# Kernel optimization log

Hardware: AMD Instinct MI355X
Metric: run time of the kernel (lower is better)

## Reference

```python
import jax, jax.numpy as jnp
import numpy as np

# Static config matching init_kwargs
COUT, CIN, K = 64, 64, 3
PAD = K // 2  # padding=1


def setup_inputs() -> dict:
    key = jax.random.key(0)
    k1, k2, k3 = jax.random.split(key, 3)
    B, H, W, FH, FW, SC = 2, 256, 256, 16, 16, 128
    hyper_params = COUT * CIN * K * K  # 36864
    x = jax.random.normal(k1, (B, CIN, H, W), jnp.float32)
    s = jax.random.normal(k2, (B, SC, FH, FW), jnp.float32)
    s2w = jax.random.normal(k3, (hyper_params, SC), jnp.float32) * 0.02
    return {"x": x, "s": s, "s2w": s2w}


def reference(x, s, s2w):
    """HyperPatchConv2d forward: per-patch dynamically generated 3x3 conv.

    x:   [b, c, h, w]   input feature map
    s:   [b, sc, fh, fw] hypernetwork signal (one vector per patch)
    s2w: [P, sc]         signal2weights 1x1 conv (P = out*cin*k*k)
    """
    b, c, h, w = x.shape
    fh, fw = s.shape[-2:]
    ph, pw = h // fh, w // fw          # patch size
    kh, kw = ph + 2 * PAD, pw + 2 * PAD  # unfold window (patch + halo)

    # signal2weights: 1x1 conv -> per-patch flattened conv weight
    wflat = jnp.einsum('pc,bcfg->bfgp', s2w, s)            # [b,fh,fw,P]
    Wdyn = wflat.reshape(b, fh, fw, COUT, CIN, K, K)        # per-patch conv kernels

    # reflect-pad then unfold into overlapping (kh,kw) patches, stride (ph,pw)
    xp = jnp.pad(x, ((0, 0), (0, 0), (PAD, PAD), (PAD, PAD)), mode='reflect')
    idx_h = (jnp.arange(fh) * ph)[:, None] + jnp.arange(kh)[None, :]  # [fh,kh]
    idx_w = (jnp.arange(fw) * pw)[:, None] + jnp.arange(kw)[None, :]  # [fw,kw]
    patches = xp[:, :, idx_h][:, :, :, :, idx_w]            # [b,c,fh,kh,fw,kw]

    # extract KxK sliding windows inside each patch (valid conv, stride 1)
    wi = jnp.arange(ph)[:, None] + jnp.arange(K)[None, :]   # [ph,K]
    wj = jnp.arange(pw)[:, None] + jnp.arange(K)[None, :]   # [pw,K]
    win = patches[:, :, :, wi]                              # [b,c,fh,ph,K,fw,kw]
    win = win[:, :, :, :, :, :, wj]                         # [b,c,fh,ph,K,fw,pw,K]
    win = win.transpose(0, 2, 5, 1, 3, 4, 6, 7)             # [b,fh,fw,c,ph,K,pw,K]

    # per-patch dynamic conv
    out = jnp.einsum('bfgocij,bfgcpiqj->bfgopq', Wdyn, win)  # [b,fh,fw,o,ph,pw]

    # fold: non-overlapping reassembly (stride == patch size)
    return out.transpose(0, 3, 1, 4, 2, 5).reshape(b, COUT, h, w)
```

## Files before the change

### kernel.cpp

```cpp
#include <hip/hip_runtime.h>
#include <hip/hip_bf16.h>


#define C_OUT 64
#define C_IN  64
#define P_TOTAL 36864
#define N_PATCH 512
#define WSTR 72
#define CSTR2 136

typedef __bf16 bf16x8 __attribute__((ext_vector_type(8)));
typedef float  f32x4  __attribute__((ext_vector_type(4)));

__device__ __forceinline__ unsigned short f2bf(float f) {
  unsigned int u = __float_as_uint(f);
  u += 0x7fffu + ((u >> 16) & 1u);
  return (unsigned short)(u >> 16);
}
__device__ __forceinline__ unsigned int pack2(float a, float b) {
  return (unsigned int)f2bf(a) | ((unsigned int)f2bf(b) << 16);
}
__device__ __forceinline__ void gll16(const void* g, void* l) {
  __builtin_amdgcn_global_load_lds(
      (const __attribute__((address_space(1))) void*)g,
      (__attribute__((address_space(3))) void*)l, 16, 0, 0);
}

__global__ __launch_bounds__(256) void prep_all(
    const float* __restrict__ x, const float* __restrict__ s, const float* __restrict__ s2w,
    unsigned short* __restrict__ xT, unsigned short* __restrict__ sTg,
    unsigned short* __restrict__ s2wP) {
  __shared__ unsigned short xl[64 * 260];
  const int bid = blockIdx.x;
  const int t = threadIdx.x;

  if (bid < 32) {
    const int sb = bid >> 4;
    const int g = bid & 15;
    float v[8];
    #pragma unroll
    for (int e = 0; e < 8; ++e)
      v[e] = s[((size_t)(sb * 128 + g * 8 + e)) * 256 + t];
    uint4 o;
    o.x = pack2(v[0], v[1]); o.y = pack2(v[2], v[3]);
    o.z = pack2(v[4], v[5]); o.w = pack2(v[6], v[7]);
    const int ntile = sb * 2 + (t >> 7);
    const int slot = (t & 127) ^ (g & 7);
    *(uint4*)(sTg + ((size_t)(ntile * 2048 + g * 128 + slot)) * 8) = o;
    return;
  }

  if (bid < 544) {
    const int b2 = bid - 32;
    const int bb = b2 >> 8, row = b2 & 255;
    #pragma unroll
    for (int it = 0; it < 16; ++it) {
      const int ci = it * 4 + (t >> 6);
      const int px = (t & 63) * 4;
      const float4 v = *(const float4*)(x + ((size_t)(bb * 64 + ci)) * 65536 + row * 256 + px);
      ushort4 o;
      o.x = f2bf(v.x); o.y = f2bf(v.y); o.z = f2bf(v.z); o.w = f2bf(v.w);
      *(ushort4*)&xl[ci * 260 + px] = o;
    }
    __syncthreads();
    unsigned short* dst = xT + ((size_t)((bb << 16) + (row << 8) + t)) * 64;
    #pragma unroll
    for (int k8 = 0; k8 < 8; ++k8) {
      const unsigned int w0 = (unsigned int)xl[(k8 * 8 + 0) * 260 + t] |
                              ((unsigned int)xl[(k8 * 8 + 1) * 260 + t] << 16);
      const unsigned int w1 = (unsigned int)xl[(k8 * 8 + 2) * 260 + t] |
                              ((unsigned int)xl[(k8 * 8 + 3) * 260 + t] << 16);
      const unsigned int w2 = (unsigned int)xl[(k8 * 8 + 4) * 260 + t] |
                              ((unsigned int)xl[(k8 * 8 + 5) * 260 + t] << 16);
      const unsigned int w3 = (unsigned int)xl[(k8 * 8 + 6) * 260 + t] |
                              ((unsigned int)xl[(k8 * 8 + 7) * 260 + t] << 16);
      *(uint4*)(dst + k8 * 8) = make_uint4(w0, w1, w2, w3);
    }
    return;
  }

  const int b3 = bid - 544;
  const int m = b3 * 64 + (t >> 2);
  const int q = t & 3;
  const int j = m & 7;
  const int lane6 = (m >> 3) & 63;
  const int fragidx = m >> 9;
  const int tap = fragidx >> 3;
  const int ksH = (fragidx >> 2) & 1;
  const int mtH = fragidx & 3;
  const int co = mtH * 16 + (lane6 & 15);
  const int ci = ksH * 32 + (lane6 >> 4) * 8 + j;
  const int p = co * 576 + ci * 9 + tap;
  const float* src = s2w + (size_t)p * 128 + q * 32;
  const int mtile = m >> 7;
  const int r128 = m & 127;
  #pragma unroll
  for (int gg = 0; gg < 4; ++gg) {
    const int g = q * 4 + gg;
    const float4 v0 = *(const float4*)(src + gg * 8);
    const float4 v1 = *(const float4*)(src + gg * 8 + 4);
    uint4 o;
    o.x = pack2(v0.x, v0.y); o.y = pack2(v0.z, v0.w);
    o.z = pack2(v1.x, v1.y); o.w = pack2(v1.z, v1.w);
    const int slot = r128 ^ (g & 7);
    *(uint4*)(s2wP + ((size_t)(mtile * 2048 + g * 128 + slot)) * 8) = o;
  }
}

__global__ __launch_bounds__(256) void wgen_kernel(
    const unsigned short* __restrict__ s2wP,
    const unsigned short* __restrict__ sTg,
    unsigned short* __restrict__ wout)
{
  __shared__ unsigned short lds[32768];
  unsigned short* As = lds;
  unsigned short* Bs = lds + 16384;
  const int tid = threadIdx.x;
  const int m0 = blockIdx.x * 128;
  const int n0 = blockIdx.y * 128;

  const unsigned short* srcA = s2wP + ((size_t)blockIdx.x) * 16384;
  const unsigned short* srcB = sTg + ((size_t)blockIdx.y) * 16384;
  #pragma unroll
  for (int i = 0; i < 8; ++i)
    gll16(srcA + (size_t)(i * 256 + tid) * 8, As + (i * 256 + tid) * 8);
  #pragma unroll
  for (int i = 0; i < 8; ++i)
    gll16(srcB + (size_t)(i * 256 + tid) * 8, Bs + (i * 256 + tid) * 8);
  __syncthreads();

  const int w = tid >> 6;
  const int lane = tid & 63;
  const int col = lane & 15;
  const int quad = lane >> 4;

  f32x4 acc[2][8] = {};
  #pragma unroll
  for (int ks = 0; ks < 4; ++ks) {
    const int g = ks * 4 + quad;
    const int gb = g * 1024;
    const int gx = (g & 7) * 8;
    bf16x8 afr[2], bfr[8];
    #pragma unroll
    for (int mti = 0; mti < 2; ++mti)
      afr[mti] = *(const bf16x8*)&As[gb + ((((w * 2 + mti) * 16 + col) * 8) ^ gx)];
    #pragma unroll
    for (int nt = 0; nt < 8; ++nt)
      bfr[nt] = *(const bf16x8*)&Bs[gb + (((nt * 16 + col) * 8) ^ gx)];
    #pragma unroll
    for (int mti = 0; mti < 2; ++mti)
      #pragma unroll
      for (int nt = 0; nt < 8; ++nt)
        acc[mti][nt] = __builtin_amdgcn_mfma_f32_16x16x32_bf16(afr[mti], bfr[nt], acc[mti][nt], 0, 0, 0);
  }
  __syncthreads();

  unsigned short* Ct = lds;
  #pragma unroll
  for (int mti = 0; mti < 2; ++mti) {
    const int mloc = (w * 2 + mti) * 16 + quad * 4;
    #pragma unroll
    for (int nt = 0; nt < 8; ++nt) {
      const int pl = nt * 16 + col;
      ushort4 o;
      o.x = f2bf(acc[mti][nt][0]); o.y = f2bf(acc[mti][nt][1]);
      o.z = f2bf(acc[mti][nt][2]); o.w = f2bf(acc[mti][nt][3]);
      *(ushort4*)&Ct[pl * CSTR2 + mloc] = o;
    }
  }
  __syncthreads();
  #pragma unroll
  for (int i = 0; i < 8; ++i) {
    const int chunk = i * 256 + tid;
    const int pl = chunk >> 4;
    const int ii = chunk & 15;
    const uint4 v = *(const uint4*)&Ct[pl * CSTR2 + ii * 8];
    *(uint4*)(wout + (size_t)(n0 + pl) * P_TOTAL + m0 + ii * 8) = v;
  }
}

__global__ __launch_bounds__(512) void conv_kernel(
    const unsigned short* __restrict__ xT,
    const unsigned short* __restrict__ wfrag,
    float* __restrict__ out)
{
  __shared__ unsigned short win[324 * WSTR];
  const int tid = threadIdx.x;
  const int patch = blockIdx.x;
  const int bb = patch >> 8;
  const int fg = patch & 255;
  const int f = fg >> 4, g = fg & 15;
  const int row0 = f * 16, col0 = g * 16;

  for (int chunk = tid; chunk < 2592; chunk += 512) {
    const int cell = chunk >> 3;
    const int j = chunk & 7;
    const int r = cell / 18;
    const int c = cell - r * 18;
    int rr = row0 + r - 1; rr = rr < 0 ? -rr : (rr > 255 ? 510 - rr : rr);
    int cc = col0 + c - 1; cc = cc < 0 ? -cc : (cc > 255 ? 510 - cc : cc);
    *(uint4*)&win[cell * WSTR + j * 8] =
        *(const uint4*)(xT + ((size_t)((bb << 16) + (rr << 8) + cc)) * 64 + j * 8);
  }
  __syncthreads();

  const int wave = tid >> 6;
  const int lane = tid & 63;
  const int t = lane & 15;
  const int quad = lane >> 4;
  const int mh = wave & 1;
  const int rq = wave >> 1;

  f32x4 acc[2][4] = {};
  const bf16x8* wb = (const bf16x8*)(wfrag + (size_t)patch * P_TOTAL);

  #pragma unroll
  for (int tap = 0; tap < 9; ++tap) {
    const int ti = tap / 3;
    const int tj = tap - ti * 3;
    bf16x8 afr[2][2];
    #pragma unroll
    for (int ks = 0; ks < 2; ++ks)
      #pragma unroll
      for (int ml = 0; ml < 2; ++ml)
        afr[ks][ml] = wb[((tap * 2 + ks) * 4 + mh * 2 + ml) * 64 + lane];

    #pragma unroll
    for (int nt = 0; nt < 4; ++nt) {
      const int r = rq * 4 + nt + ti;
      const int c = t + tj;
      const int base = (r * 18 + c) * WSTR + quad * 8;
      #pragma unroll
      for (int ks = 0; ks < 2; ++ks) {
        const bf16x8 bfr = *(const bf16x8*)&win[base + ks * 32];
        acc[0][nt] = __builtin_amdgcn_mfma_f32_16x16x32_bf16(afr[ks][0], bfr, acc[0][nt], 0, 0, 0);
        acc[1][nt] = __builtin_amdgcn_mfma_f32_16x16x32_bf16(afr[ks][1], bfr, acc[1][nt], 0, 0, 0);
      }
    }
  }

  #pragma unroll
  for (int ml = 0; ml < 2; ++ml) {
    #pragma unroll
    for (int nt = 0; nt < 4; ++nt) {
      const int p = row0 + rq * 4 + nt;
      #pragma unroll
      for (int reg = 0; reg < 4; ++reg) {
        const int co = (mh * 2 + ml) * 16 + quad * 4 + reg;
        out[(((size_t)bb * C_OUT + co) << 16) + ((size_t)p << 8) + col0 + t] = acc[ml][nt][reg];
      }
    }
  }
}

extern "C" void kernel_launch(void* const* d_in, const int* in_sizes, int n_in,
                              void* d_out, int out_size, void* d_ws, size_t ws_size,
                              hipStream_t stream) {
  const float* x   = (const float*)d_in[0];
  const float* s   = (const float*)d_in[1];
  const float* s2w = (const float*)d_in[2];
  float* out = (float*)d_out;

  char* ws = (char*)d_ws;
  unsigned short* wbuf = (unsigned short*)(ws);
  unsigned short* sTg  = (unsigned short*)(ws + 37748736);
  unsigned short* xT   = (unsigned short*)(ws + 37879808);
  unsigned short* s2wP = (unsigned short*)(ws + 54657024);

  prep_all<<<1120, 256, 0, stream>>>(x, s, s2w, xT, sTg, s2wP);
  wgen_kernel<<<dim3(288, 4), 256, 0, stream>>>(s2wP, sTg, wbuf);
  conv_kernel<<<N_PATCH, 512, 0, stream>>>(xT, wbuf, out);
}
```

Baseline: 132.1 us.

## Fuse prep, weight generation and conv into one cooperative kernel with grid syncs

Merges the three launches into a single cooperative kernel of 512 blocks that uses grid-wide syncs between the prep, weight-generation GEMM and per-patch conv phases. It falls back to the old three-kernel path if occupancy or the cooperative launch fails. The aim is to remove launch gaps and tail effects between kernels. In exchange it adds two grid barriers, runs the GEMM phase with 512 blocks looping over 1152 tiles (previously 1152 separate blocks) and uses a larger workgroup. It also calls an occupancy query on the host every launch.

```diff
diff --git a/kernel.cpp b/kernel.cpp
--- a/kernel.cpp
+++ b/kernel.cpp
@@ -1,5 +1,8 @@
 #include <hip/hip_runtime.h>
 #include <hip/hip_bf16.h>
+#include <hip/hip_cooperative_groups.h>
+
+namespace cg = cooperative_groups;
 
 
 #define C_OUT 64
@@ -24,6 +27,225 @@
   __builtin_amdgcn_global_load_lds(
       (const __attribute__((address_space(1))) void*)g,
       (__attribute__((address_space(3))) void*)l, 16, 0, 0);
+}
+
+__global__ __launch_bounds__(512, 4) void fused_kernel(
+    const float* __restrict__ x, const float* __restrict__ s, const float* __restrict__ s2w,
+    unsigned short* __restrict__ xT, unsigned short* __restrict__ sTg,
+    unsigned short* __restrict__ s2wP, unsigned short* __restrict__ wbuf,
+    float* __restrict__ out)
+{
+  __shared__ unsigned short lds[32768];
+  cg::grid_group grid = cg::this_grid();
+  const int bid = blockIdx.x;
+  const int tid = threadIdx.x;
+
+  {
+    const int bb = bid >> 8, row = bid & 255;
+    unsigned short* xl = lds;
+    #pragma unroll
+    for (int it = 0; it < 8; ++it) {
+      const int ci = it * 8 + (tid >> 6);
+      const int px = (tid & 63) * 4;
+      const float4 v = *(const float4*)(x + ((size_t)(bb * 64 + ci)) * 65536 + row * 256 + px);
+      ushort4 o;
+      o.x = f2bf(v.x); o.y = f2bf(v.y); o.z = f2bf(v.z); o.w = f2bf(v.w);
+      *(ushort4*)&xl[ci * 260 + px] = o;
+    }
+    __syncthreads();
+    const int px = tid & 255;
+    const int k8h = (tid >> 8) * 4;
+    unsigned short* dst = xT + ((size_t)((bb << 16) + (row << 8) + px)) * 64;
+    #pragma unroll
+    for (int k8i = 0; k8i < 4; ++k8i) {
+      const int k8 = k8h + k8i;
+      const unsigned int w0 = (unsigned int)xl[(k8 * 8 + 0) * 260 + px] |
+                              ((unsigned int)xl[(k8 * 8 + 1) * 260 + px] << 16);
+      const unsigned int w1 = (unsigned int)xl[(k8 * 8 + 2) * 260 + px] |
+                              ((unsigned int)xl[(k8 * 8 + 3) * 260 + px] << 16);
+      const unsigned int w2 = (unsigned int)xl[(k8 * 8 + 4) * 260 + px] |
+                              ((unsigned int)xl[(k8 * 8 + 5) * 260 + px] << 16);
+      const unsigned int w3 = (unsigned int)xl[(k8 * 8 + 6) * 260 + px] |
+                              ((unsigned int)xl[(k8 * 8 + 7) * 260 + px] << 16);
+      *(uint4*)(dst + k8 * 8) = make_uint4(w0, w1, w2, w3);
+    }
+  }
+  if (bid < 288) {
+    const int m = bid * 128 + (tid >> 2);
+    const int q = tid & 3;
+    const int j = m & 7;
+    const int lane6 = (m >> 3) & 63;
+    const int fragidx = m >> 9;
+    const int tap = fragidx >> 3;
+    const int ksH = (fragidx >> 2) & 1;
+    const int mtH = fragidx & 3;
+    const int co = mtH * 16 + (lane6 & 15);
+    const int ci = ksH * 32 + (lane6 >> 4) * 8 + j;
+    const int p = co * 576 + ci * 9 + tap;
+    const float* src = s2w + (size_t)p * 128 + q * 32;
+    const int mtile = m >> 7;
+    const int r128 = m & 127;
+    #pragma unroll
+    for (int gg = 0; gg < 4; ++gg) {
+      const int g = q * 4 + gg;
+      const float4 v0 = *(const float4*)(src + gg * 8);
+      const float4 v1 = *(const float4*)(src + gg * 8 + 4);
+      uint4 o;
+      o.x = pack2(v0.x, v0.y); o.y = pack2(v0.z, v0.w);
+      o.z = pack2(v1.x, v1.y); o.w = pack2(v1.z, v1.w);
+      const int slot = r128 ^ (g & 7);
+      *(uint4*)(s2wP + ((size_t)(mtile * 2048 + g * 128 + slot)) * 8) = o;
+    }
+  } else if (bid < 304) {
+    const int u = bid - 288;
+    const int sb = u >> 3;
+    const int g = ((u & 7) << 1) | (tid >> 8);
+    const int t = tid & 255;
+    float v[8];
+    #pragma unroll
+    for (int e = 0; e < 8; ++e)
+      v[e] = s[((size_t)(sb * 128 + g * 8 + e)) * 256 + t];
+    uint4 o;
+    o.x = pack2(v[0], v[1]); o.y = pack2(v[2], v[3]);
+    o.z = pack2(v[4], v[5]); o.w = pack2(v[6], v[7]);
+    const int ntile = sb * 2 + (t >> 7);
+    const int slot = (t & 127) ^ (g & 7);
+    *(uint4*)(sTg + ((size_t)(ntile * 2048 + g * 128 + slot)) * 8) = o;
+  }
+  __threadfence();
+  grid.sync();
+
+  {
+    unsigned short* As = lds;
+    unsigned short* Bs = lds + 16384;
+    const int w = tid >> 6;
+    const int lane = tid & 63;
+    const int col = lane & 15;
+    const int quad = lane >> 4;
+    for (int tile = bid; tile < 1152; tile += 512) {
+      const int n = tile / 288;
+      const int mt = tile - n * 288;
+      const unsigned short* srcA = s2wP + (size_t)mt * 16384;
+      const unsigned short* srcB = sTg + (size_t)n * 16384;
+      #pragma unroll
+      for (int i = 0; i < 4; ++i)
+        gll16(srcA + (size_t)(i * 512 + tid) * 8, As + (i * 512 + tid) * 8);
+      #pragma unroll
+      for (int i = 0; i < 4; ++i)
+        gll16(srcB + (size_t)(i * 512 + tid) * 8, Bs + (i * 512 + tid) * 8);
+      __syncthreads();
+
+      f32x4 acc[8] = {};
+      #pragma unroll
+      for (int ks = 0; ks < 4; ++ks) {
+        const int g = ks * 4 + quad;
+        const int gb = g * 1024;
+        const int gx = (g & 7) * 8;
+        const bf16x8 afr = *(const bf16x8*)&As[gb + (((w * 16 + col) * 8) ^ gx)];
+        bf16x8 bfr[8];
+        #pragma unroll
+        for (int nt = 0; nt < 8; ++nt)
+          bfr[nt] = *(const bf16x8*)&Bs[gb + (((nt * 16 + col) * 8) ^ gx)];
+        #pragma unroll
+        for (int nt = 0; nt < 8; ++nt)
+          acc[nt] = __builtin_amdgcn_mfma_f32_16x16x32_bf16(afr, bfr[nt], acc[nt], 0, 0, 0);
+      }
+      __syncthreads();
+
+      unsigned short* Ct = lds;
+      const int mloc = w * 16 + quad * 4;
+      #pragma unroll
+      for (int nt = 0; nt < 8; ++nt) {
+        const int pl = nt * 16 + col;
+        ushort4 o;
+        o.x = f2bf(acc[nt][0]); o.y = f2bf(acc[nt][1]);
+        o.z = f2bf(acc[nt][2]); o.w = f2bf(acc[nt][3]);
+        *(ushort4*)&Ct[pl * CSTR2 + mloc] = o;
+      }
+      __syncthreads();
+      const int m0 = mt * 128, n0 = n * 128;
+      #pragma unroll
+      for (int i = 0; i < 4; ++i) {
+        const int chunk = i * 512 + tid;
+        const int pl = chunk >> 4;
+        const int ii = chunk & 15;
+        const uint4 v = *(const uint4*)&Ct[pl * CSTR2 + ii * 8];
+        *(uint4*)(wbuf + (size_t)(n0 + pl) * P_TOTAL + m0 + ii * 8) = v;
+      }
+      __syncthreads();
+    }
+  }
+  __threadfence();
+  grid.sync();
+
+  {
+    unsigned short* win = lds;
+    const int patch = bid;
+    const int bb = patch >> 8;
+    const int fg = patch & 255;
+    const int f = fg >> 4, g = fg & 15;
+    const int row0 = f * 16, col0 = g * 16;
+
+    for (int chunk = tid; chunk < 2592; chunk += 512) {
+      const int cell = chunk >> 3;
+      const int j = chunk & 7;
+      const int r = cell / 18;
+      const int c = cell - r * 18;
+      int rr = row0 + r - 1; rr = rr < 0 ? -rr : (rr > 255 ? 510 - rr : rr);
+      int cc = col0 + c - 1; cc = cc < 0 ? -cc : (cc > 255 ? 510 - cc : cc);
+      *(uint4*)&win[cell * WSTR + j * 8] =
+          *(const uint4*)(xT + ((size_t)((bb << 16) + (rr << 8) + cc)) * 64 + j * 8);
+    }
+    __syncthreads();
+
+    const int wave = tid >> 6;
+    const int lane = tid & 63;
+    const int t = lane & 15;
+    const int quad = lane >> 4;
+    const int mh = wave & 1;
+    const int rq = wave >> 1;
+
+    f32x4 acc[2][4] = {};
+    const bf16x8* wb = (const bf16x8*)(wbuf + (size_t)patch * P_TOTAL);
+
+    #pragma unroll
+    for (int tap = 0; tap < 9; ++tap) {
+      const int ti = tap / 3;
+      const int tj = tap - ti * 3;
+      bf16x8 afr[2][2];
+      #pragma unroll
+      for (int ks = 0; ks < 2; ++ks)
+        #pragma unroll
+        for (int ml = 0; ml < 2; ++ml)
+          afr[ks][ml] = wb[((tap * 2 + ks) * 4 + mh * 2 + ml) * 64 + lane];
+
+      #pragma unroll
+      for (int nt = 0; nt < 4; ++nt) {
+        const int r = rq * 4 + nt + ti;
+        const int c = t + tj;
+        const int base = (r * 18 + c) * WSTR + quad * 8;
+        #pragma unroll
+        for (int ks = 0; ks < 2; ++ks) {
+          const bf16x8 bfr = *(const bf16x8*)&win[base + ks * 32];
+          acc[0][nt] = __builtin_amdgcn_mfma_f32_16x16x32_bf16(afr[ks][0], bfr, acc[0][nt], 0, 0, 0);
+          acc[1][nt] = __builtin_amdgcn_mfma_f32_16x16x32_bf16(afr[ks][1], bfr, acc[1][nt], 0, 0, 0);
+        }
+      }
+    }
+
+    #pragma unroll
+    for (int ml = 0; ml < 2; ++ml) {
+      #pragma unroll
+      for (int nt = 0; nt < 4; ++nt) {
+        const int p = row0 + rq * 4 + nt;
+        #pragma unroll
+        for (int reg = 0; reg < 4; ++reg) {
+          const int co = (mh * 2 + ml) * 16 + quad * 4 + reg;
+          out[(((size_t)bb * C_OUT + co) << 16) + ((size_t)p << 8) + col0 + t] = acc[ml][nt][reg];
+        }
+      }
+    }
+  }
 }
 
 __global__ __launch_bounds__(256) void prep_all(
@@ -108,8 +330,7 @@
 }
 
 __global__ __launch_bounds__(256) void wgen_kernel(
-    const unsigned short* __restrict__ s2wP,
-    const unsigned short* __restrict__ sTg,
+    const unsigned short* __restrict__ s2wP, const unsigned short* __restrict__ sTg,
     unsigned short* __restrict__ wout)
 {
   __shared__ unsigned short lds[32768];
@@ -180,8 +401,7 @@
 }
 
 __global__ __launch_bounds__(512) void conv_kernel(
-    const unsigned short* __restrict__ xT,
-    const unsigned short* __restrict__ wfrag,
+    const unsigned short* __restrict__ xT, const unsigned short* __restrict__ wfrag,
     float* __restrict__ out)
 {
   __shared__ unsigned short win[324 * WSTR];
@@ -267,7 +487,18 @@
   unsigned short* xT   = (unsigned short*)(ws + 37879808);
   unsigned short* s2wP = (unsigned short*)(ws + 54657024);
 
-  prep_all<<<1120, 256, 0, stream>>>(x, s, s2w, xT, sTg, s2wP);
-  wgen_kernel<<<dim3(288, 4), 256, 0, stream>>>(s2wP, sTg, wbuf);
-  conv_kernel<<<N_PATCH, 512, 0, stream>>>(xT, wbuf, out);
-}
+  int maxB = 0;
+  hipError_t qe = hipOccupancyMaxActiveBlocksPerMultiprocessor(&maxB, fused_kernel, 512, 0);
+  bool coop_ok = (qe == hipSuccess && maxB >= 2);
+  if (coop_ok) {
+    void* kargs[] = {(void*)&x, (void*)&s, (void*)&s2w, (void*)&xT,
+                     (void*)&sTg, (void*)&s2wP, (void*)&wbuf, (void*)&out};
+    coop_ok = (hipLaunchCooperativeKernel(fused_kernel, dim3(512), dim3(512),
+                                          kargs, 0, stream) == hipSuccess);
+  }
+  if (!coop_ok) {
+    prep_all<<<1120, 256, 0, stream>>>(x, s, s2w, xT, sTg, s2wP);
+    wgen_kernel<<<dim3(288, 4), 256, 0, stream>>>(s2wP, sTg, wbuf);
+    conv_kernel<<<N_PATCH, 512, 0, stream>>>(xT, wbuf, out);
+  }
+}
```

Result: no change. 133.3 us (+0.9%).

## Move x transpose into weight-generation launch and cap conv kernel at two blocks

Applied to the files above, without the earlier changes.

Splits the preprocessing kernel so it only packs s and s2w, and moves the x-to-bf16 channel-last transpose into the weight-generation GEMM launch as extra blocks. The x transpose then runs alongside the GEMM tiles rather than ahead of them in the prep kernel, which shortens the critical path of the prep stage. The GEMM blocks now use a flattened 1D grid. Separately, conv_kernel gets a min-blocks launch bound of 2, which may limit registers and could cause spills.

```diff
diff --git a/kernel.cpp b/kernel.cpp
--- a/kernel.cpp
+++ b/kernel.cpp
@@ -26,11 +26,9 @@
       (__attribute__((address_space(3))) void*)l, 16, 0, 0);
 }
 
-__global__ __launch_bounds__(256) void prep_all(
-    const float* __restrict__ x, const float* __restrict__ s, const float* __restrict__ s2w,
-    unsigned short* __restrict__ xT, unsigned short* __restrict__ sTg,
-    unsigned short* __restrict__ s2wP) {
-  __shared__ unsigned short xl[64 * 260];
+__global__ __launch_bounds__(256) void prep_ws(
+    const float* __restrict__ s, const float* __restrict__ s2w,
+    unsigned short* __restrict__ sTg, unsigned short* __restrict__ s2wP) {
   const int bid = blockIdx.x;
   const int t = threadIdx.x;
 
@@ -50,36 +48,7 @@
     return;
   }
 
-  if (bid < 544) {
-    const int b2 = bid - 32;
-    const int bb = b2 >> 8, row = b2 & 255;
-    #pragma unroll
-    for (int it = 0; it < 16; ++it) {
-      const int ci = it * 4 + (t >> 6);
-      const int px = (t & 63) * 4;
-      const float4 v = *(const float4*)(x + ((size_t)(bb * 64 + ci)) * 65536 + row * 256 + px);
-      ushort4 o;
-      o.x = f2bf(v.x); o.y = f2bf(v.y); o.z = f2bf(v.z); o.w = f2bf(v.w);
-      *(ushort4*)&xl[ci * 260 + px] = o;
-    }
-    __syncthreads();
-    unsigned short* dst = xT + ((size_t)((bb << 16) + (row << 8) + t)) * 64;
-    #pragma unroll
-    for (int k8 = 0; k8 < 8; ++k8) {
-      const unsigned int w0 = (unsigned int)xl[(k8 * 8 + 0) * 260 + t] |
-                              ((unsigned int)xl[(k8 * 8 + 1) * 260 + t] << 16);
-      const unsigned int w1 = (unsigned int)xl[(k8 * 8 + 2) * 260 + t] |
-                              ((unsigned int)xl[(k8 * 8 + 3) * 260 + t] << 16);
-      const unsigned int w2 = (unsigned int)xl[(k8 * 8 + 4) * 260 + t] |
-                              ((unsigned int)xl[(k8 * 8 + 5) * 260 + t] << 16);
-      const unsigned int w3 = (unsigned int)xl[(k8 * 8 + 6) * 260 + t] |
-                              ((unsigned int)xl[(k8 * 8 + 7) * 260 + t] << 16);
-      *(uint4*)(dst + k8 * 8) = make_uint4(w0, w1, w2, w3);
-    }
-    return;
-  }
-
-  const int b3 = bid - 544;
+  const int b3 = bid - 32;
   const int m = b3 * 64 + (t >> 2);
   const int q = t & 3;
   const int j = m & 7;
@@ -107,20 +76,56 @@
   }
 }
 
-__global__ __launch_bounds__(256) void wgen_kernel(
+__global__ __launch_bounds__(256) void wgen_plus(
+    const float* __restrict__ x,
     const unsigned short* __restrict__ s2wP,
     const unsigned short* __restrict__ sTg,
+    unsigned short* __restrict__ xT,
     unsigned short* __restrict__ wout)
 {
   __shared__ unsigned short lds[32768];
+  const int bid = blockIdx.x;
+  const int tid = threadIdx.x;
+
+  if (bid < 512) {
+    const int bb = bid >> 8, row = bid & 255;
+    unsigned short* xl = lds;
+    #pragma unroll
+    for (int it = 0; it < 16; ++it) {
+      const int ci = it * 4 + (tid >> 6);
+      const int px = (tid & 63) * 4;
+      const float4 v = *(const float4*)(x + ((size_t)(bb * 64 + ci)) * 65536 + row * 256 + px);
+      ushort4 o;
+      o.x = f2bf(v.x); o.y = f2bf(v.y); o.z = f2bf(v.z); o.w = f2bf(v.w);
+      *(ushort4*)&xl[ci * 260 + px] = o;
+    }
+    __syncthreads();
+    unsigned short* dst = xT + ((size_t)((bb << 16) + (row << 8) + tid)) * 64;
+    #pragma unroll
+    for (int k8 = 0; k8 < 8; ++k8) {
+      const unsigned int w0 = (unsigned int)xl[(k8 * 8 + 0) * 260 + tid] |
+                              ((unsigned int)xl[(k8 * 8 + 1) * 260 + tid] << 16);
+      const unsigned int w1 = (unsigned int)xl[(k8 * 8 + 2) * 260 + tid] |
+                              ((unsigned int)xl[(k8 * 8 + 3) * 260 + tid] << 16);
+      const unsigned int w2 = (unsigned int)xl[(k8 * 8 + 4) * 260 + tid] |
+                              ((unsigned int)xl[(k8 * 8 + 5) * 260 + tid] << 16);
+      const unsigned int w3 = (unsigned int)xl[(k8 * 8 + 6) * 260 + tid] |
+                              ((unsigned int)xl[(k8 * 8 + 7) * 260 + tid] << 16);
+      *(uint4*)(dst + k8 * 8) = make_uint4(w0, w1, w2, w3);
+    }
+    return;
+  }
+
+  const int bid2 = bid - 512;
+  const int n = bid2 / 288;
+  const int mt = bid2 - n * 288;
+  const int m0 = mt * 128;
+  const int n0 = n * 128;
   unsigned short* As = lds;
   unsigned short* Bs = lds + 16384;
-  const int tid = threadIdx.x;
-  const int m0 = blockIdx.x * 128;
-  const int n0 = blockIdx.y * 128;
-
-  const unsigned short* srcA = s2wP + ((size_t)blockIdx.x) * 16384;
-  const unsigned short* srcB = sTg + ((size_t)blockIdx.y) * 16384;
+
+  const unsigned short* srcA = s2wP + (size_t)mt * 16384;
+  const unsigned short* srcB = sTg + (size_t)n * 16384;
   #pragma unroll
   for (int i = 0; i < 8; ++i)
     gll16(srcA + (size_t)(i * 256 + tid) * 8, As + (i * 256 + tid) * 8);
@@ -179,7 +184,7 @@
   }
 }
 
-__global__ __launch_bounds__(512) void conv_kernel(
+__global__ __launch_bounds__(512, 2) void conv_kernel(
     const unsigned short* __restrict__ xT,
     const unsigned short* __restrict__ wfrag,
     float* __restrict__ out)
@@ -267,7 +272,7 @@
   unsigned short* xT   = (unsigned short*)(ws + 37879808);
   unsigned short* s2wP = (unsigned short*)(ws + 54657024);
 
-  prep_all<<<1120, 256, 0, stream>>>(x, s, s2w, xT, sTg, s2wP);
-  wgen_kernel<<<dim3(288, 4), 256, 0, stream>>>(s2wP, sTg, wbuf);
+  prep_ws<<<608, 256, 0, stream>>>(s, s2w, sTg, s2wP);
+  wgen_plus<<<1664, 256, 0, stream>>>(x, s2wP, sTg, xT, wbuf);
   conv_kernel<<<N_PATCH, 512, 0, stream>>>(xT, wbuf, out);
 }
```

Result: faster. 129.0 us (-2.3%).
